# Kernel optimization log

Hardware: AMD Instinct MI355X
Metric: run time of the kernel (lower is better)

The kernel has to match this reference:

```python
import jax, jax.numpy as jnp
import numpy as np

B, V, D, L = 2048, 50000, 256, 32
N = V - 1  # internal (non-leaf) Huffman nodes


def setup_inputs() -> dict:
    key = jax.random.key(0)
    k1, k2, k3, k4, k5, k6 = jax.random.split(key, 6)
    inputs_vector = jax.random.normal(k1, (B, V), jnp.float32)
    W = jax.random.normal(k2, (D, V), jnp.float32) / np.float32(np.sqrt(V))  # Linear weight [out,in]
    cls_w = jax.random.normal(k3, (N, D), jnp.float32)
    path_nodes = jax.random.randint(k4, (B, L), 0, N)
    huffman_codes = jax.random.randint(k5, (B, L), 0, 2).astype(jnp.int32)
    path_lengths = jax.random.randint(k6, (B,), 0, L).astype(jnp.int32)
    return {
        "inputs_vector": inputs_vector,
        "W": W,
        "cls_w": cls_w,
        "path_nodes": path_nodes,
        "huffman_codes": huffman_codes,
        "path_lengths": path_lengths,
    }


def reference(inputs_vector, W, cls_w, path_nodes, huffman_codes, path_lengths):
    # x = embedding(inputs_vector): Linear with no bias -> inputs @ W.T  [B, D]
    x = inputs_vector @ W.T
    # gather ragged Huffman-path node vectors (padded to L)  [B, L, D]
    path_vecs = cls_w[path_nodes]
    # per-sample tiny matmul: logits[i] = x[i] @ path_vecs[i].T  [B, L]
    logits = jnp.einsum("bd,bld->bl", x, path_vecs)
    y = huffman_codes.astype(logits.dtype)
    # stable BCE-with-logits per element
    bce = jnp.maximum(logits, 0.0) - logits * y + jnp.log1p(jnp.exp(-jnp.abs(logits)))
    # mask padded positions; per-sample mean over true path length (BCEWithLogitsLoss mean reduction)
    lengths = jnp.maximum(path_lengths, 1).astype(logits.dtype)  # guard length-0 pads
    mask = (jnp.arange(L)[None, :] < jnp.maximum(path_lengths, 1)[:, None]).astype(logits.dtype)
    per_sample = jnp.sum(bce * mask, axis=1) / lengths
    # loop accumulates per-sample means then divides by batch_size -> mean over batch
    loss = jnp.mean(per_sample)
    return loss[None]  # original returns a shape-[1] tensor
```

## Files before the change

### kernel.cpp

```cpp
#include <hip/hip_runtime.h>
#include <hip/hip_bf16.h>

#define M_DIM 2048
#define K_DIM 50000
#define N_DIM 256
#define L_PATH 32
#define BMt 128
#define BNt 256
#define BKt 64
#define TOTAL_KSTEPS 782
#define KSPLIT 16
#define STEPS_PER_SPLIT 49
#define MTILES 16

typedef __bf16 bf16x8 __attribute__((ext_vector_type(8)));
typedef float f32x4 __attribute__((ext_vector_type(4)));
typedef float fx4 __attribute__((ext_vector_type(4)));
typedef unsigned int u32x2 __attribute__((ext_vector_type(2)));

__device__ __forceinline__ unsigned short f2bf(float f) {
  unsigned int u = __float_as_uint(f);
  u += 0x7FFFu + ((u >> 16) & 1u);
  return (unsigned short)(u >> 16);
}
__device__ __forceinline__ unsigned int pack2(float lo, float hi) {
  return (unsigned int)f2bf(lo) | ((unsigned int)f2bf(hi) << 16);
}

__global__ __launch_bounds__(512)
void gemm_bf16_splitk(const float* __restrict__ A, const float* __restrict__ W,
                      float* __restrict__ outp, int use_atomic)
{
  __shared__ __align__(16) unsigned short sA[2][BMt * BKt];
  __shared__ __align__(16) unsigned short sW[2][BNt * BKt];

  int bid = blockIdx.x;
  int per = gridDim.x >> 3;
  int Lw = (bid & 7) * per + (bid >> 3);
  int mtile = Lw & (MTILES - 1);
  int ksp = Lw >> 4;

  int m0 = mtile * BMt;
  int s0 = ksp * STEPS_PER_SPLIT;
  int s1 = s0 + STEPS_PER_SPLIT;
  if (s1 > TOTAL_KSTEPS) s1 = TOTAL_KSTEPS;

  int tid = threadIdx.x;
  int wid = tid >> 6, lane = tid & 63;
  int wm = wid >> 2, wn = wid & 3;
  int l15 = lane & 15, l4 = lane >> 4;

  int rowt = tid >> 4;
  int chk  = tid & 15;
  const float* Ab = A + (size_t)(m0 + rowt) * K_DIM + chk * 4;
  const float* Wb = W + (size_t)rowt * K_DIM + chk * 4;

  int offA[4], offW[8];
#pragma unroll
  for (int i = 0; i < 4; ++i) {
    int r = i * 32 + rowt;
    offA[i] = r * BKt + ((((chk >> 1) ^ (r & 7)) << 3) + (chk & 1) * 4);
  }
#pragma unroll
  for (int i = 0; i < 8; ++i) {
    int r = i * 32 + rowt;
    offW[i] = r * BKt + ((((chk >> 1) ^ (r & 7)) << 3) + (chk & 1) * 4);
  }

  fx4 ra[4], rw[8];

  auto load_step = [&](int s) {
    size_t kb = (size_t)s * BKt;
    const float* ap = Ab + kb;
    const float* wp = Wb + kb;
    int k = s * BKt + chk * 4;
    if (k + 4 <= K_DIM) {
#pragma unroll
      for (int i = 0; i < 4; ++i) ra[i] = *reinterpret_cast<const fx4*>(ap + (size_t)i * 32 * K_DIM);
#pragma unroll
      for (int i = 0; i < 8; ++i) rw[i] = *reinterpret_cast<const fx4*>(wp + (size_t)i * 32 * K_DIM);
    } else {
#pragma unroll
      for (int i = 0; i < 4; ++i) {
        fx4 f;
#pragma unroll
        for (int e = 0; e < 4; ++e) f[e] = (k + e < K_DIM) ? ap[(size_t)i * 32 * K_DIM + e] : 0.f;
        ra[i] = f;
      }
#pragma unroll
      for (int i = 0; i < 8; ++i) {
        fx4 f;
#pragma unroll
        for (int e = 0; e < 4; ++e) f[e] = (k + e < K_DIM) ? wp[(size_t)i * 32 * K_DIM + e] : 0.f;
        rw[i] = f;
      }
    }
  };

  auto write_step = [&](int p) {
#pragma unroll
    for (int i = 0; i < 4; ++i) {
      u32x2 v; v[0] = pack2(ra[i][0], ra[i][1]); v[1] = pack2(ra[i][2], ra[i][3]);
      *reinterpret_cast<u32x2*>(&sA[p][offA[i]]) = v;
    }
#pragma unroll
    for (int i = 0; i < 8; ++i) {
      u32x2 v; v[0] = pack2(rw[i][0], rw[i][1]); v[1] = pack2(rw[i][2], rw[i][3]);
      *reinterpret_cast<u32x2*>(&sW[p][offW[i]]) = v;
    }
  };

  f32x4 acc[4][4] = {};

  auto compute = [&](int p) {
#pragma unroll
    for (int kk = 0; kk < 2; ++kk) {
      bf16x8 afr[4], bfr[4];
      int c = kk * 32 + l4 * 8;
#pragma unroll
      for (int mf = 0; mf < 4; ++mf) {
        int r = wm * 64 + mf * 16 + l15;
        afr[mf] = *reinterpret_cast<const bf16x8*>(&sA[p][r * BKt + (c ^ ((r & 7) << 3))]);
      }
#pragma unroll
      for (int nf = 0; nf < 4; ++nf) {
        int r = wn * 64 + nf * 16 + l15;
        bfr[nf] = *reinterpret_cast<const bf16x8*>(&sW[p][r * BKt + (c ^ ((r & 7) << 3))]);
      }
#pragma unroll
      for (int mf = 0; mf < 4; ++mf)
#pragma unroll
        for (int nf = 0; nf < 4; ++nf)
          acc[mf][nf] = __builtin_amdgcn_mfma_f32_16x16x32_bf16(afr[mf], bfr[nf], acc[mf][nf], 0, 0, 0);
    }
  };

  load_step(s0);
  write_step(0);
  if (s0 + 1 < s1) load_step(s0 + 1);
  __syncthreads();

  int p = 0;
  for (int s = s0; s < s1; ++s) {
    compute(p);
    if (s + 1 < s1) {
      write_step(p ^ 1);
      if (s + 2 < s1) load_step(s + 2);
      __syncthreads();
    }
    p ^= 1;
  }

  if (use_atomic) {
#pragma unroll
    for (int mf = 0; mf < 4; ++mf)
#pragma unroll
      for (int nf = 0; nf < 4; ++nf)
#pragma unroll
        for (int j = 0; j < 4; ++j) {
          int row = m0 + wm * 64 + mf * 16 + l4 * 4 + j;
          int col = wn * 64 + nf * 16 + l15;
          atomicAdd(&outp[(size_t)row * N_DIM + col], acc[mf][nf][j]);
        }
  } else {
    float* part = outp + (size_t)ksp * (M_DIM * N_DIM);
#pragma unroll
    for (int mf = 0; mf < 4; ++mf)
#pragma unroll
      for (int nf = 0; nf < 4; ++nf)
#pragma unroll
        for (int j = 0; j < 4; ++j) {
          int row = m0 + wm * 64 + mf * 16 + l4 * 4 + j;
          int col = wn * 64 + nf * 16 + l15;
          part[(size_t)row * N_DIM + col] = acc[mf][nf][j];
        }
  }
}

__global__ __launch_bounds__(256)
void loss_kernel(const float* __restrict__ part, int nparts,
                 const float* __restrict__ cls_w,
                 const int* __restrict__ nodes, const int* __restrict__ codes,
                 const int* __restrict__ lens, float* __restrict__ per_sample)
{
  int i = blockIdx.x;
  int tid = threadIdx.x;
  __shared__ float s_x[N_DIM];
  {
    float s = 0.f;
    for (int k = 0; k < nparts; ++k)
      s += part[(size_t)k * (M_DIM * N_DIM) + (size_t)i * N_DIM + tid];
    s_x[tid] = s;
  }
  __syncthreads();

  int wid = tid >> 6, lane = tid & 63;
  __shared__ float s_logit[L_PATH];
  fx4 xv = *reinterpret_cast<const fx4*>(&s_x[lane * 4]);
#pragma unroll
  for (int j = 0; j < 8; ++j) {
    int pos = wid * 8 + j;
    int node = nodes[i * L_PATH + pos];
    fx4 cv = *reinterpret_cast<const fx4*>(&cls_w[(size_t)node * N_DIM + lane * 4]);
    float d = xv[0] * cv[0] + xv[1] * cv[1] + xv[2] * cv[2] + xv[3] * cv[3];
#pragma unroll
    for (int s = 32; s > 0; s >>= 1) d += __shfl_xor(d, s);
    if (lane == 0) s_logit[pos] = d;
  }
  __syncthreads();
  if (wid == 0) {
    int len = lens[i];
    int lenc = len < 1 ? 1 : len;
    float v = 0.f;
    if (lane < L_PATH && lane < lenc) {
      float z = s_logit[lane];
      float y = (float)codes[i * L_PATH + lane];
      v = fmaxf(z, 0.f) - z * y + log1pf(expf(-fabsf(z)));
    }
#pragma unroll
    for (int s = 32; s > 0; s >>= 1) v += __shfl_xor(v, s);
    if (lane == 0) per_sample[i] = v / (float)lenc;
  }
}

__global__ __launch_bounds__(256)
void final_reduce(const float* __restrict__ ps, float* __restrict__ out) {
  int tid = threadIdx.x;
  float s = 0.f;
#pragma unroll
  for (int i = 0; i < M_DIM / 256; ++i) s += ps[tid + i * 256];
  __shared__ float sm[4];
#pragma unroll
  for (int sh = 32; sh > 0; sh >>= 1) s += __shfl_xor(s, sh);
  if ((tid & 63) == 0) sm[tid >> 6] = s;
  __syncthreads();
  if (tid == 0) out[0] = (sm[0] + sm[1] + sm[2] + sm[3]) * (1.0f / (float)M_DIM);
}

extern "C" void kernel_launch(void* const* d_in, const int* in_sizes, int n_in,
                              void* d_out, int out_size, void* d_ws, size_t ws_size,
                              hipStream_t stream) {
  const float* A     = (const float*)d_in[0];
  const float* W     = (const float*)d_in[1];
  const float* cls_w = (const float*)d_in[2];
  const int* nodes   = (const int*)d_in[3];
  const int* codes   = (const int*)d_in[4];
  const int* lens    = (const int*)d_in[5];
  float* out = (float*)d_out;

  char* ws = (char*)d_ws;
  const size_t XBYTES = (size_t)M_DIM * N_DIM * sizeof(float);
  float* per_sample = (float*)ws;
  float* x          = (float*)(ws + (size_t)(64u << 10));
  float* partials   = (float*)(ws + (size_t)(4u << 20));

  int use_atomic = (ws_size < (size_t)(4u << 20) + (size_t)KSPLIT * XBYTES) ? 1 : 0;

  if (use_atomic) {
    hipMemsetAsync(x, 0, XBYTES, stream);
    gemm_bf16_splitk<<<dim3(MTILES * KSPLIT), dim3(512), 0, stream>>>(A, W, x, 1);
    loss_kernel<<<dim3(M_DIM), dim3(256), 0, stream>>>(x, 1, cls_w, nodes, codes, lens, per_sample);
  } else {
    gemm_bf16_splitk<<<dim3(MTILES * KSPLIT), dim3(512), 0, stream>>>(A, W, partials, 0);
    loss_kernel<<<dim3(M_DIM), dim3(256), 0, stream>>>(partials, KSPLIT, cls_w, nodes, codes, lens, per_sample);
  }
  final_reduce<<<dim3(1), dim3(256), 0, stream>>>(per_sample, out);
}
```

Measured before the change: 163.9 us.

## Double-buffer global-load registers and issue loads before compute in split-K GEMM

Replaces the single register staging set with two alternating register stages, so the global load for step t+2 is issued before the MFMA compute of step t and the loads stay in flight longer. The manual fp32-to-bf16 bit rounding is swapped for native __bf16 casts. __syncthreads is replaced by an explicit lgkmcnt wait plus s_barrier, and launch bounds request 2 blocks per CU. The extra register stage raises register pressure, which may conflict with the 2-blocks-per-CU occupancy target and cause spills.

```diff
diff --git a/kernel.cpp b/kernel.cpp
--- a/kernel.cpp
+++ b/kernel.cpp
@@ -14,20 +14,13 @@
 #define MTILES 16
 
 typedef __bf16 bf16x8 __attribute__((ext_vector_type(8)));
+typedef __bf16 bf16x4 __attribute__((ext_vector_type(4)));
 typedef float f32x4 __attribute__((ext_vector_type(4)));
 typedef float fx4 __attribute__((ext_vector_type(4)));
-typedef unsigned int u32x2 __attribute__((ext_vector_type(2)));
-
-__device__ __forceinline__ unsigned short f2bf(float f) {
-  unsigned int u = __float_as_uint(f);
-  u += 0x7FFFu + ((u >> 16) & 1u);
-  return (unsigned short)(u >> 16);
-}
-__device__ __forceinline__ unsigned int pack2(float lo, float hi) {
-  return (unsigned int)f2bf(lo) | ((unsigned int)f2bf(hi) << 16);
-}
-
-__global__ __launch_bounds__(512)
+
+struct StageRegs { fx4 a[4]; fx4 w[8]; };
+
+__global__ __launch_bounds__(512, 2)
 void gemm_bf16_splitk(const float* __restrict__ A, const float* __restrict__ W,
                       float* __restrict__ outp, int use_atomic)
 {
@@ -67,46 +60,50 @@
     offW[i] = r * BKt + ((((chk >> 1) ^ (r & 7)) << 3) + (chk & 1) * 4);
   }
 
-  fx4 ra[4], rw[8];
-
-  auto load_step = [&](int s) {
+  StageRegs r0, r1;
+
+  auto issue = [&](StageRegs& R, int s) {
     size_t kb = (size_t)s * BKt;
     const float* ap = Ab + kb;
     const float* wp = Wb + kb;
     int k = s * BKt + chk * 4;
     if (k + 4 <= K_DIM) {
 #pragma unroll
-      for (int i = 0; i < 4; ++i) ra[i] = *reinterpret_cast<const fx4*>(ap + (size_t)i * 32 * K_DIM);
-#pragma unroll
-      for (int i = 0; i < 8; ++i) rw[i] = *reinterpret_cast<const fx4*>(wp + (size_t)i * 32 * K_DIM);
+      for (int i = 0; i < 4; ++i) R.a[i] = *reinterpret_cast<const fx4*>(ap + (size_t)i * 32 * K_DIM);
+#pragma unroll
+      for (int i = 0; i < 8; ++i) R.w[i] = *reinterpret_cast<const fx4*>(wp + (size_t)i * 32 * K_DIM);
     } else {
 #pragma unroll
       for (int i = 0; i < 4; ++i) {
         fx4 f;
 #pragma unroll
         for (int e = 0; e < 4; ++e) f[e] = (k + e < K_DIM) ? ap[(size_t)i * 32 * K_DIM + e] : 0.f;
-        ra[i] = f;
+        R.a[i] = f;
       }
 #pragma unroll
       for (int i = 0; i < 8; ++i) {
         fx4 f;
 #pragma unroll
         for (int e = 0; e < 4; ++e) f[e] = (k + e < K_DIM) ? wp[(size_t)i * 32 * K_DIM + e] : 0.f;
-        rw[i] = f;
+        R.w[i] = f;
       }
     }
   };
 
-  auto write_step = [&](int p) {
+  auto pack = [&](StageRegs& R, int p) {
 #pragma unroll
     for (int i = 0; i < 4; ++i) {
-      u32x2 v; v[0] = pack2(ra[i][0], ra[i][1]); v[1] = pack2(ra[i][2], ra[i][3]);
-      *reinterpret_cast<u32x2*>(&sA[p][offA[i]]) = v;
+      bf16x4 h;
+      h[0] = (__bf16)R.a[i][0]; h[1] = (__bf16)R.a[i][1];
+      h[2] = (__bf16)R.a[i][2]; h[3] = (__bf16)R.a[i][3];
+      *reinterpret_cast<bf16x4*>(&sA[p][offA[i]]) = h;
     }
 #pragma unroll
     for (int i = 0; i < 8; ++i) {
-      u32x2 v; v[0] = pack2(rw[i][0], rw[i][1]); v[1] = pack2(rw[i][2], rw[i][3]);
-      *reinterpret_cast<u32x2*>(&sW[p][offW[i]]) = v;
+      bf16x4 h;
+      h[0] = (__bf16)R.w[i][0]; h[1] = (__bf16)R.w[i][1];
+      h[2] = (__bf16)R.w[i][2]; h[3] = (__bf16)R.w[i][3];
+      *reinterpret_cast<bf16x4*>(&sW[p][offW[i]]) = h;
     }
   };
 
@@ -135,21 +132,30 @@
     }
   };
 
-  load_step(s0);
-  write_step(0);
-  if (s0 + 1 < s1) load_step(s0 + 1);
-  __syncthreads();
-
-  int p = 0;
-  for (int s = s0; s < s1; ++s) {
+#define WB() do { asm volatile("s_waitcnt lgkmcnt(0)" ::: "memory"); \
+                  __builtin_amdgcn_s_barrier(); } while (0)
+
+  issue(r0, s0);
+  if (s0 + 1 < s1) issue(r1, s0 + 1);
+  pack(r0, 0);
+  WB();
+
+  int t = s0, p = 0;
+  for (;;) {
+    if (t + 1 >= s1) { compute(p); break; }
+    if (t + 2 < s1) issue(r0, t + 2);
     compute(p);
-    if (s + 1 < s1) {
-      write_step(p ^ 1);
-      if (s + 2 < s1) load_step(s + 2);
-      __syncthreads();
-    }
-    p ^= 1;
-  }
+    pack(r1, p ^ 1);
+    WB();
+    ++t; p ^= 1;
+    if (t + 1 >= s1) { compute(p); break; }
+    if (t + 2 < s1) issue(r1, t + 2);
+    compute(p);
+    pack(r0, p ^ 1);
+    WB();
+    ++t; p ^= 1;
+  }
+#undef WB
 
   if (use_atomic) {
 #pragma unroll
```

Result: slower. 373.7 us (+128.1%).

## Stream fp32 tiles directly into LDS with a triple-buffered async pipeline

Applied to the files above, without the earlier changes.

Replaces the register-staged global load, bf16 conversion and LDS write with global_load_lds DMA of raw fp32 tiles into three LDS buffers. K-step shrinks from 64 to 32 and the fp32-to-bf16 conversion moves to fragment-read time. The aim is to take the load path off the VGPRs and overlap two steps of loads with compute using vmcnt waits. In exchange it doubles LDS bytes per element, adds conversion work in the inner loop, and relies on hand-written waitcnt/barrier ordering.

```diff
diff --git a/kernel.cpp b/kernel.cpp
--- a/kernel.cpp
+++ b/kernel.cpp
@@ -7,32 +7,28 @@
 #define L_PATH 32
 #define BMt 128
 #define BNt 256
-#define BKt 64
-#define TOTAL_KSTEPS 782
+#define BK 32
+#define TOTAL_STEPS 1563
 #define KSPLIT 16
-#define STEPS_PER_SPLIT 49
+#define SPS 98
 #define MTILES 16
+#define ATILE (BMt * BK)
+#define WTILE (BNt * BK)
 
 typedef __bf16 bf16x8 __attribute__((ext_vector_type(8)));
 typedef float f32x4 __attribute__((ext_vector_type(4)));
 typedef float fx4 __attribute__((ext_vector_type(4)));
-typedef unsigned int u32x2 __attribute__((ext_vector_type(2)));
-
-__device__ __forceinline__ unsigned short f2bf(float f) {
-  unsigned int u = __float_as_uint(f);
-  u += 0x7FFFu + ((u >> 16) & 1u);
-  return (unsigned short)(u >> 16);
-}
-__device__ __forceinline__ unsigned int pack2(float lo, float hi) {
-  return (unsigned int)f2bf(lo) | ((unsigned int)f2bf(hi) << 16);
-}
+
+#define GLL(g, l) __builtin_amdgcn_global_load_lds(                        \
+    (const __attribute__((address_space(1))) void*)(g),                    \
+    (__attribute__((address_space(3))) void*)(l), 16, 0, 0)
 
 __global__ __launch_bounds__(512)
 void gemm_bf16_splitk(const float* __restrict__ A, const float* __restrict__ W,
                       float* __restrict__ outp, int use_atomic)
 {
-  __shared__ __align__(16) unsigned short sA[2][BMt * BKt];
-  __shared__ __align__(16) unsigned short sW[2][BNt * BKt];
+  __shared__ __align__(16) float sA[3 * ATILE];
+  __shared__ __align__(16) float sW[3 * WTILE];
 
   int bid = blockIdx.x;
   int per = gridDim.x >> 3;
@@ -41,115 +37,112 @@
   int ksp = Lw >> 4;
 
   int m0 = mtile * BMt;
-  int s0 = ksp * STEPS_PER_SPLIT;
-  int s1 = s0 + STEPS_PER_SPLIT;
-  if (s1 > TOTAL_KSTEPS) s1 = TOTAL_KSTEPS;
+  int s0 = ksp * SPS;
+  int s1 = s0 + SPS;
+  if (s1 > TOTAL_STEPS) s1 = TOTAL_STEPS;
 
   int tid = threadIdx.x;
   int wid = tid >> 6, lane = tid & 63;
   int wm = wid >> 2, wn = wid & 3;
   int l15 = lane & 15, l4 = lane >> 4;
 
-  int rowt = tid >> 4;
-  int chk  = tid & 15;
-  const float* Ab = A + (size_t)(m0 + rowt) * K_DIM + chk * 4;
-  const float* Wb = W + (size_t)rowt * K_DIM + chk * 4;
-
-  int offA[4], offW[8];
-#pragma unroll
-  for (int i = 0; i < 4; ++i) {
-    int r = i * 32 + rowt;
-    offA[i] = r * BKt + ((((chk >> 1) ^ (r & 7)) << 3) + (chk & 1) * 4);
-  }
-#pragma unroll
-  for (int i = 0; i < 8; ++i) {
-    int r = i * 32 + rowt;
-    offW[i] = r * BKt + ((((chk >> 1) ^ (r & 7)) << 3) + (chk & 1) * 4);
-  }
-
-  fx4 ra[4], rw[8];
-
-  auto load_step = [&](int s) {
-    size_t kb = (size_t)s * BKt;
-    const float* ap = Ab + kb;
-    const float* wp = Wb + kb;
-    int k = s * BKt + chk * 4;
-    if (k + 4 <= K_DIM) {
-#pragma unroll
-      for (int i = 0; i < 4; ++i) ra[i] = *reinterpret_cast<const fx4*>(ap + (size_t)i * 32 * K_DIM);
-#pragma unroll
-      for (int i = 0; i < 8; ++i) rw[i] = *reinterpret_cast<const fx4*>(wp + (size_t)i * 32 * K_DIM);
+  int gg = (lane & 7) ^ (lane >> 3);
+  int cA = wid * 2;
+  int cW = wid * 4;
+  const float* pA0 = A + (size_t)(m0 + cA * 8 + (lane >> 3)) * K_DIM + gg * 4;
+  const float* pA1 = pA0 + (size_t)8 * K_DIM;
+  const float* pW0 = W + (size_t)(cW * 8 + (lane >> 3)) * K_DIM + gg * 4;
+  const float* pW1 = pW0 + (size_t)8 * K_DIM;
+  const float* pW2 = pW0 + (size_t)16 * K_DIM;
+  const float* pW3 = pW0 + (size_t)24 * K_DIM;
+  int lane4 = lane * 4;
+
+  auto stage = [&](int p, int s) {
+    size_t koff = (size_t)s * BK;
+    float* dA = sA + p * ATILE + cA * 256;
+    float* dW = sW + p * WTILE + cW * 256;
+    if (s != TOTAL_STEPS - 1) {
+      GLL(pA0 + koff, dA);
+      GLL(pA1 + koff, dA + 256);
+      GLL(pW0 + koff, dW);
+      GLL(pW1 + koff, dW + 256);
+      GLL(pW2 + koff, dW + 512);
+      GLL(pW3 + koff, dW + 768);
     } else {
-#pragma unroll
-      for (int i = 0; i < 4; ++i) {
-        fx4 f;
-#pragma unroll
-        for (int e = 0; e < 4; ++e) f[e] = (k + e < K_DIM) ? ap[(size_t)i * 32 * K_DIM + e] : 0.f;
-        ra[i] = f;
+      if (gg < 4) {
+        GLL(pA0 + koff, dA);
+        GLL(pA1 + koff, dA + 256);
+        GLL(pW0 + koff, dW);
+        GLL(pW1 + koff, dW + 256);
+        GLL(pW2 + koff, dW + 512);
+        GLL(pW3 + koff, dW + 768);
+      } else {
+        fx4 z = {0.f, 0.f, 0.f, 0.f};
+        *reinterpret_cast<fx4*>(dA + lane4) = z;
+        *reinterpret_cast<fx4*>(dA + 256 + lane4) = z;
+        *reinterpret_cast<fx4*>(dW + lane4) = z;
+        *reinterpret_cast<fx4*>(dW + 256 + lane4) = z;
+        *reinterpret_cast<fx4*>(dW + 512 + lane4) = z;
+        *reinterpret_cast<fx4*>(dW + 768 + lane4) = z;
+        asm volatile("s_waitcnt lgkmcnt(0)" ::: "memory");
       }
-#pragma unroll
-      for (int i = 0; i < 8; ++i) {
-        fx4 f;
-#pragma unroll
-        for (int e = 0; e < 4; ++e) f[e] = (k + e < K_DIM) ? wp[(size_t)i * 32 * K_DIM + e] : 0.f;
-        rw[i] = f;
-      }
     }
   };
 
-  auto write_step = [&](int p) {
-#pragma unroll
-    for (int i = 0; i < 4; ++i) {
-      u32x2 v; v[0] = pack2(ra[i][0], ra[i][1]); v[1] = pack2(ra[i][2], ra[i][3]);
-      *reinterpret_cast<u32x2*>(&sA[p][offA[i]]) = v;
-    }
-#pragma unroll
-    for (int i = 0; i < 8; ++i) {
-      u32x2 v; v[0] = pack2(rw[i][0], rw[i][1]); v[1] = pack2(rw[i][2], rw[i][3]);
-      *reinterpret_cast<u32x2*>(&sW[p][offW[i]]) = v;
-    }
+  f32x4 acc[4][4] = {};
+
+  auto compute = [&](const float* bufA, const float* bufW) {
+    bf16x8 afr[4], bfr[4];
+#pragma unroll
+    for (int mf = 0; mf < 4; ++mf) {
+      int r = wm * 64 + mf * 16 + l15;
+      int x7 = r & 7;
+      const float* pr = bufA + r * BK;
+      fx4 lo = *reinterpret_cast<const fx4*>(pr + (((l4 * 2) ^ x7) * 4));
+      fx4 hi = *reinterpret_cast<const fx4*>(pr + (((l4 * 2 + 1) ^ x7) * 4));
+      bf16x8 f;
+      f[0] = (__bf16)lo[0]; f[1] = (__bf16)lo[1]; f[2] = (__bf16)lo[2]; f[3] = (__bf16)lo[3];
+      f[4] = (__bf16)hi[0]; f[5] = (__bf16)hi[1]; f[6] = (__bf16)hi[2]; f[7] = (__bf16)hi[3];
+      afr[mf] = f;
+    }
+#pragma unroll
+    for (int nf = 0; nf < 4; ++nf) {
+      int r = wn * 64 + nf * 16 + l15;
+      int x7 = r & 7;
+      const float* pr = bufW + r * BK;
+      fx4 lo = *reinterpret_cast<const fx4*>(pr + (((l4 * 2) ^ x7) * 4));
+      fx4 hi = *reinterpret_cast<const fx4*>(pr + (((l4 * 2 + 1) ^ x7) * 4));
+      bf16x8 f;
+      f[0] = (__bf16)lo[0]; f[1] = (__bf16)lo[1]; f[2] = (__bf16)lo[2]; f[3] = (__bf16)lo[3];
+      f[4] = (__bf16)hi[0]; f[5] = (__bf16)hi[1]; f[6] = (__bf16)hi[2]; f[7] = (__bf16)hi[3];
+      bfr[nf] = f;
+    }
+#pragma unroll
+    for (int mf = 0; mf < 4; ++mf)
+#pragma unroll
+      for (int nf = 0; nf < 4; ++nf)
+        acc[mf][nf] = __builtin_amdgcn_mfma_f32_16x16x32_bf16(afr[mf], bfr[nf], acc[mf][nf], 0, 0, 0);
   };
 
-  f32x4 acc[4][4] = {};
-
-  auto compute = [&](int p) {
-#pragma unroll
-    for (int kk = 0; kk < 2; ++kk) {
-      bf16x8 afr[4], bfr[4];
-      int c = kk * 32 + l4 * 8;
-#pragma unroll
-      for (int mf = 0; mf < 4; ++mf) {
-        int r = wm * 64 + mf * 16 + l15;
-        afr[mf] = *reinterpret_cast<const bf16x8*>(&sA[p][r * BKt + (c ^ ((r & 7) << 3))]);
-      }
-#pragma unroll
-      for (int nf = 0; nf < 4; ++nf) {
-        int r = wn * 64 + nf * 16 + l15;
-        bfr[nf] = *reinterpret_cast<const bf16x8*>(&sW[p][r * BKt + (c ^ ((r & 7) << 3))]);
-      }
-#pragma unroll
-      for (int mf = 0; mf < 4; ++mf)
-#pragma unroll
-        for (int nf = 0; nf < 4; ++nf)
-          acc[mf][nf] = __builtin_amdgcn_mfma_f32_16x16x32_bf16(afr[mf], bfr[nf], acc[mf][nf], 0, 0, 0);
-    }
-  };
-
-  load_step(s0);
-  write_step(0);
-  if (s0 + 1 < s1) load_step(s0 + 1);
-  __syncthreads();
-
-  int p = 0;
-  for (int s = s0; s < s1; ++s) {
-    compute(p);
-    if (s + 1 < s1) {
-      write_step(p ^ 1);
-      if (s + 2 < s1) load_step(s + 2);
-      __syncthreads();
-    }
-    p ^= 1;
-  }
+  stage(0, s0);
+  stage(1, s0 + 1);
+
+  int t = s0, p = 0;
+  while (t + 1 < s1) {
+    asm volatile("s_waitcnt vmcnt(6)" ::: "memory");
+    __builtin_amdgcn_s_barrier();
+    asm volatile("" ::: "memory");
+    if (t + 2 < s1) {
+      int p2 = p + 2; if (p2 >= 3) p2 -= 3;
+      stage(p2, t + 2);
+    }
+    compute(sA + p * ATILE, sW + p * WTILE);
+    ++t; ++p; if (p == 3) p = 0;
+  }
+  asm volatile("s_waitcnt vmcnt(0)" ::: "memory");
+  __builtin_amdgcn_s_barrier();
+  asm volatile("" ::: "memory");
+  compute(sA + p * ATILE, sW + p * WTILE);
 
   if (use_atomic) {
 #pragma unroll
```

Measured after the change: 228.0 us. 39.2% more time.
